# Kernel optimization log

Hardware: AMD Instinct MI355X
Metric: run time of the kernel (lower is better)

Reference implementation:

```python
import jax, jax.numpy as jnp
import numpy as np

N_NODES = 100000
N_EDGES = 1600000
IN_CH = 128


def _sage_conv(x, src, dst, Wl, b, Wr, n_nodes):
    # PyG SAGEConv (aggr='mean', root_weight=True):
    #   out_i = lin_l(mean_{j->i} x_j) + lin_r(x_i)
    msg = x[src]                                             # [E, F]
    agg = jax.ops.segment_sum(msg, dst, num_segments=n_nodes)  # [N, F]
    deg = jax.ops.segment_sum(jnp.ones((src.shape[0],), x.dtype), dst,
                              num_segments=n_nodes)          # [N]
    mean = agg / jnp.maximum(deg, 1.0)[:, None]
    return mean @ Wl + b + x @ Wr


def setup_inputs() -> dict:
    key = jax.random.key(0)
    ks = jax.random.split(key, 10)
    x = jax.random.normal(ks[0], (N_NODES, IN_CH), dtype=jnp.float32)
    edge_index = jax.random.randint(ks[1], (2, N_EDGES), 0, N_NODES, dtype=jnp.int64)
    s = 0.05
    return {
        "x": x,
        "edge_index": edge_index,
        "W1l": jax.random.normal(ks[2], (IN_CH, 32), dtype=jnp.float32) * s,
        "b1": jax.random.normal(ks[3], (32,), dtype=jnp.float32) * s,
        "W1r": jax.random.normal(ks[4], (IN_CH, 32), dtype=jnp.float32) * s,
        "W2l": jax.random.normal(ks[5], (32, 16), dtype=jnp.float32) * s,
        "b2": jax.random.normal(ks[6], (16,), dtype=jnp.float32) * s,
        "W2r": jax.random.normal(ks[7], (32, 16), dtype=jnp.float32) * s,
        "Wfc": jax.random.normal(ks[8], (16, 2), dtype=jnp.float32) * s,
        "bfc": jax.random.normal(ks[9], (2,), dtype=jnp.float32) * s,
    }


def reference(x, edge_index, W1l, b1, W1r, W2l, b2, W2r, Wfc, bfc):
    src, dst = edge_index[0], edge_index[1]
    n = x.shape[0]
    h = jax.nn.relu(_sage_conv(x, src, dst, W1l, b1, W1r, n))   # [N, 32]
    h = jax.nn.relu(_sage_conv(h, src, dst, W2l, b2, W2r, n))   # [N, 16]
    return h @ Wfc + bfc                                        # [N, 2]
```

## Files before the change

### kernel.cpp

```cpp
#include <hip/hip_runtime.h>

#define TPB 256
#define BK_SHIFT 7
#define BK_SIZE 128
#define NBK_MAX 784
#define CAP 2816
#define SC_EPB 4096
#define GEMM_BLKS 1024

typedef __attribute__((ext_vector_type(8))) short bf16x8;
typedef __attribute__((ext_vector_type(4))) float f32x4;
typedef __attribute__((ext_vector_type(2))) float f32x2;
typedef __attribute__((ext_vector_type(4))) unsigned short u16x4;

__device__ __forceinline__ unsigned short f2bf(float f) {
    unsigned u = __float_as_uint(f);
    unsigned r = (u + 0x7FFFu + ((u >> 16) & 1u)) >> 16;
    return (unsigned short)r;
}
__device__ __forceinline__ float bf2f(unsigned short b) {
    return __uint_as_float((unsigned)b << 16);
}
__device__ __forceinline__ void acc4(f32x4& a, u16x4 v) {
    a.x += bf2f(v.x); a.y += bf2f(v.y); a.z += bf2f(v.z); a.w += bf2f(v.w);
}
__device__ __forceinline__ unsigned char f2fp8(float f) {
    int p = __builtin_amdgcn_cvt_pk_fp8_f32(f, f, 0, false);
    return (unsigned char)(p & 0xFF);
}
__device__ __forceinline__ void acc4f8(f32x4& a, unsigned u) {
    f32x2 lo = __builtin_amdgcn_cvt_pk_f32_fp8(u, false);
    f32x2 hi = __builtin_amdgcn_cvt_pk_f32_fp8(u, true);
    a.x += lo.x; a.y += lo.y; a.z += hi.x; a.w += hi.y;
}
__device__ __forceinline__ void gload_lds16(const void* g, void* l) {
    __builtin_amdgcn_global_load_lds(
        (const __attribute__((address_space(1))) void*)g,
        (__attribute__((address_space(3))) void*)l, 16, 0, 0);
}

struct ScatterSmem {
    int lcnt [NBK_MAX];
    int soff [1024];
    int lbase[NBK_MAX];
    int lrank[NBK_MAX];
    int spv  [SC_EPB];
    unsigned short sbk[SC_EPB];
};
union BuildSmem {
    ScatterSmem sc;
    char xstage[4 * 8192];
};

__global__ __launch_bounds__(256) void build_and_gemm1(
    const int* __restrict__ src, const int* __restrict__ dst,
    int* __restrict__ gfill, int* __restrict__ pk, int E, int NBK, int NSC,
    const float* __restrict__ A,
    const float* __restrict__ Wl,
    const float* __restrict__ Wr,
    const float* __restrict__ b,
    unsigned char* __restrict__ Y8,
    float* __restrict__ C,
    int N)
{
    __shared__ BuildSmem smem;
    const int t = threadIdx.x;

    if ((int)blockIdx.x < NSC) {
        int* lcnt  = smem.sc.lcnt;
        int* soff  = smem.sc.soff;
        int* lbase = smem.sc.lbase;
        int* lrank = smem.sc.lrank;
        int* spv   = smem.sc.spv;
        unsigned short* sbk = smem.sc.sbk;
        const int e0 = blockIdx.x * SC_EPB;

        for (int i = t; i < NBK_MAX; i += 256) { lcnt[i] = 0; lrank[i] = 0; }
        __syncthreads();

        #pragma unroll
        for (int k = 0; k < SC_EPB / 1024; ++k) {
            int e = e0 + k * 1024 + t * 4;
            if (e < E) {
                int4 d = *(const int4*)&dst[e];
                atomicAdd(&lcnt[d.x >> BK_SHIFT], 1);
                atomicAdd(&lcnt[d.y >> BK_SHIFT], 1);
                atomicAdd(&lcnt[d.z >> BK_SHIFT], 1);
                atomicAdd(&lcnt[d.w >> BK_SHIFT], 1);
            }
        }
        __syncthreads();

        for (int i = t; i < 1024; i += 256) soff[i] = (i < NBK) ? lcnt[i] : 0;
        __syncthreads();
        for (int off = 1; off < 1024; off <<= 1) {
            int u0 = (t       >= off) ? soff[t       - off] : 0;
            int u1 = (t + 256 >= off) ? soff[t + 256 - off] : 0;
            int u2 = (t + 512 >= off) ? soff[t + 512 - off] : 0;
            int u3 = (t + 768 >= off) ? soff[t + 768 - off] : 0;
            __syncthreads();
            soff[t] += u0; soff[t + 256] += u1;
            soff[t + 512] += u2; soff[t + 768] += u3;
            __syncthreads();
        }

        for (int i = t; i < NBK; i += 256) {
            int c = lcnt[i];
            if (c) lbase[i] = atomicAdd(&gfill[i], c);
        }
        __syncthreads();

        #pragma unroll
        for (int k = 0; k < SC_EPB / 1024; ++k) {
            int e = e0 + k * 1024 + t * 4;
            if (e < E) {
                int4 d = *(const int4*)&dst[e];
                int4 s = *(const int4*)&src[e];
                {
                    int bb = d.x >> BK_SHIFT;
                    int pos = (soff[bb] - lcnt[bb]) + atomicAdd(&lrank[bb], 1);
                    spv[pos] = (s.x << BK_SHIFT) | (d.x & (BK_SIZE - 1));
                    sbk[pos] = (unsigned short)bb;
                }
                {
                    int bb = d.y >> BK_SHIFT;
                    int pos = (soff[bb] - lcnt[bb]) + atomicAdd(&lrank[bb], 1);
                    spv[pos] = (s.y << BK_SHIFT) | (d.y & (BK_SIZE - 1));
                    sbk[pos] = (unsigned short)bb;
                }
                {
                    int bb = d.z >> BK_SHIFT;
                    int pos = (soff[bb] - lcnt[bb]) + atomicAdd(&lrank[bb], 1);
                    spv[pos] = (s.z << BK_SHIFT) | (d.z & (BK_SIZE - 1));
                    sbk[pos] = (unsigned short)bb;
                }
                {
                    int bb = d.w >> BK_SHIFT;
                    int pos = (soff[bb] - lcnt[bb]) + atomicAdd(&lrank[bb], 1);
                    spv[pos] = (s.w << BK_SHIFT) | (d.w & (BK_SIZE - 1));
                    sbk[pos] = (unsigned short)bb;
                }
            }
        }
        __syncthreads();

        const int blockcnt = soff[NBK - 1];
        for (int i = t; i < blockcnt; i += 256) {
            int bb = sbk[i];
            int gpos = lbase[bb] + (i - (soff[bb] - lcnt[bb]));
            if (gpos < CAP) pk[(size_t)bb * CAP + gpos] = spv[i];
        }
        return;
    }

    const int lane = t & 63;
    const int wid  = t >> 6;
    const int m    = lane & 15;
    const int quad = lane >> 4;
    const int wave   = (blockIdx.x - NSC) * 4 + wid;
    const int nwaves = GEMM_BLKS * 4;
    const int ntiles = (N + 15) >> 4;

    char* xbuf = smem.xstage + wid * 8192;

    bf16x8 Bf[4][4];
    #pragma unroll
    for (int kc = 0; kc < 4; ++kc) {
        #pragma unroll
        for (int jt = 0; jt < 4; ++jt) {
            const float* W = (jt < 2) ? Wl : Wr;
            const int col = (jt & 1) * 16 + m;
            #pragma unroll
            for (int j = 0; j < 8; ++j) {
                int k = kc * 32 + quad * 8 + j;
                Bf[kc][jt][j] = (short)f2bf(W[k * 32 + col]);
            }
        }
    }

    const float bias0 = b[m];
    const float bias1 = b[16 + m];
    const int swz = m & 7;

    for (int tile = wave; tile < ntiles; tile += nwaves) {
        const char* xtile = (const char*)A + (size_t)tile * 8192;
        asm volatile("s_waitcnt lgkmcnt(0)" ::: "memory");
        #pragma unroll
        for (int i = 0; i < 8; ++i) {
            int o  = i * 1024 + lane * 16;
            int r  = o >> 9;
            int cs = (o & 511) >> 4;
            int c  = cs ^ (r & 7);
            gload_lds16(xtile + r * 512 + c * 16, xbuf + i * 1024);
        }
        asm volatile("s_waitcnt vmcnt(0)" ::: "memory");
        __builtin_amdgcn_sched_barrier(0);

        bf16x8 Af[4];
        #pragma unroll
        for (int kc = 0; kc < 4; ++kc) {
            const int c0 = kc * 8 + quad * 2;
            f32x4 v0 = *(const f32x4*)(xbuf + m * 512 + ((c0       ^ swz) << 4));
            f32x4 v1 = *(const f32x4*)(xbuf + m * 512 + (((c0 + 1) ^ swz) << 4));
            Af[kc][0] = (short)f2bf(v0.x); Af[kc][1] = (short)f2bf(v0.y);
            Af[kc][2] = (short)f2bf(v0.z); Af[kc][3] = (short)f2bf(v0.w);
            Af[kc][4] = (short)f2bf(v1.x); Af[kc][5] = (short)f2bf(v1.y);
            Af[kc][6] = (short)f2bf(v1.z); Af[kc][7] = (short)f2bf(v1.w);
        }

        f32x4 acc[4] = {{0.f,0.f,0.f,0.f},{0.f,0.f,0.f,0.f},
                        {0.f,0.f,0.f,0.f},{0.f,0.f,0.f,0.f}};
        #pragma unroll
        for (int kc = 0; kc < 4; ++kc) {
            #pragma unroll
            for (int jt = 0; jt < 4; ++jt)
                acc[jt] = __builtin_amdgcn_mfma_f32_16x16x32_bf16(
                    Af[kc], Bf[kc][jt], acc[jt], 0, 0, 0);
        }

        const int node0 = tile * 16;
        const int nodeBase = node0 + quad * 4;
        #pragma unroll
        for (int reg = 0; reg < 4; ++reg) {
            const int node = nodeBase + reg;
            if (node < N) {
                Y8[(size_t)node * 32 + m]      = f2fp8(acc[0][reg]);
                Y8[(size_t)node * 32 + 16 + m] = f2fp8(acc[1][reg]);
                C [(size_t)node * 32 + m]      = acc[2][reg] + bias0;
                C [(size_t)node * 32 + 16 + m] = acc[3][reg] + bias1;
            }
        }
    }
}

__global__ __launch_bounds__(256) void gather_gemm2(
    const int* __restrict__ gfill, const int* __restrict__ pk,
    const unsigned char* __restrict__ Y8,
    const float* __restrict__ c1,
    const float* __restrict__ W2l, const float* __restrict__ W2r,
    const float* __restrict__ b2,
    unsigned short* __restrict__ y2b, float* __restrict__ c2, int N)
{
    __shared__ int lcnt[BK_SIZE];
    __shared__ int soff[BK_SIZE];
    __shared__ int wcur[BK_SIZE];
    __shared__ int sidx[CAP];

    const int t = threadIdx.x;
    const int b = blockIdx.x;
    const size_t base = (size_t)b * CAP;
    const int cnt  = min(gfill[b], CAP);
    const int node0 = b * BK_SIZE;

    if (t < BK_SIZE) lcnt[t] = 0;
    __syncthreads();

    for (int j = t; j < cnt; j += 256)
        atomicAdd(&lcnt[pk[base + j] & (BK_SIZE - 1)], 1);
    __syncthreads();

    int v = (t < BK_SIZE) ? lcnt[t] : 0;
    if (t < BK_SIZE) soff[t] = v;
    __syncthreads();
    for (int off = 1; off < BK_SIZE; off <<= 1) {
        int u = (t < BK_SIZE && t >= off) ? soff[t - off] : 0;
        __syncthreads();
        if (t < BK_SIZE) soff[t] += u;
        __syncthreads();
    }
    if (t < BK_SIZE) wcur[t] = soff[t] - v;
    __syncthreads();

    for (int j = t; j < cnt; j += 256) {
        int pv = pk[base + j];
        int d  = pv & (BK_SIZE - 1);
        int pos = atomicAdd(&wcur[d], 1);
        sidx[pos] = pv >> BK_SHIFT;
    }
    __syncthreads();

    const int q = t & 7;
    #pragma unroll
    for (int pass = 0; pass < 4; ++pass) {
        const int nl = pass * 32 + (t >> 3);
        const int node = node0 + nl;
        const bool active = node < N;
        float h[4] = {0.f, 0.f, 0.f, 0.f};
        if (active) {
            const int deg = lcnt[nl];
            const int en  = soff[nl];
            const int st  = en - deg;
            const float w = 1.0f / fmaxf((float)deg, 1.0f);

            f32x4 a0 = {0.f,0.f,0.f,0.f};
            f32x4 a1 = {0.f,0.f,0.f,0.f};
            f32x4 a2 = {0.f,0.f,0.f,0.f};
            f32x4 a3 = {0.f,0.f,0.f,0.f};
            int j = st;
            for (; j + 3 < en; j += 4) {
                int s0 = sidx[j], s1 = sidx[j+1], s2 = sidx[j+2], s3 = sidx[j+3];
                unsigned u0 = *(const unsigned*)&Y8[(size_t)s0 * 32 + q * 4];
                unsigned u1 = *(const unsigned*)&Y8[(size_t)s1 * 32 + q * 4];
                unsigned u2 = *(const unsigned*)&Y8[(size_t)s2 * 32 + q * 4];
                unsigned u3 = *(const unsigned*)&Y8[(size_t)s3 * 32 + q * 4];
                acc4f8(a0, u0); acc4f8(a1, u1); acc4f8(a2, u2); acc4f8(a3, u3);
            }
            for (; j < en; ++j) {
                unsigned uu = *(const unsigned*)&Y8[(size_t)sidx[j] * 32 + q * 4];
                acc4f8(a0, uu);
            }
            f32x4 acc;
            acc.x = (a0.x + a1.x) + (a2.x + a3.x);
            acc.y = (a0.y + a1.y) + (a2.y + a3.y);
            acc.z = (a0.z + a1.z) + (a2.z + a3.z);
            acc.w = (a0.w + a1.w) + (a2.w + a3.w);

            f32x4 c = __builtin_nontemporal_load((const f32x4*)&c1[(size_t)node * 32 + q * 4]);
            h[0] = fmaxf(c.x + acc.x * w, 0.f);
            h[1] = fmaxf(c.y + acc.y * w, 0.f);
            h[2] = fmaxf(c.z + acc.z * w, 0.f);
            h[3] = fmaxf(c.w + acc.w * w, 0.f);
        }

        const int  j0  = q * 4;
        const bool isY = (j0 < 16);
        const int  jj  = isY ? j0 : (j0 - 16);
        const float* Wb = isY ? W2l : W2r;

        float o0 = 0.f, o1 = 0.f, o2 = 0.f, o3 = 0.f;
        #pragma unroll
        for (int k = 0; k < 32; ++k) {
            float hk = __shfl(h[k & 3], k >> 2, 8);
            f32x4 wv = *(const f32x4*)&Wb[k * 16 + jj];
            o0 += hk * wv.x; o1 += hk * wv.y; o2 += hk * wv.z; o3 += hk * wv.w;
        }

        if (active) {
            if (isY) {
                u16x4 r;
                r.x = f2bf(o0); r.y = f2bf(o1); r.z = f2bf(o2); r.w = f2bf(o3);
                *(u16x4*)&y2b[(size_t)node * 16 + jj] = r;
            } else {
                f32x4 bb = *(const f32x4*)&b2[jj];
                f32x4 ov = {o0 + bb.x, o1 + bb.y, o2 + bb.z, o3 + bb.w};
                __builtin_nontemporal_store(ov, (f32x4*)&c2[(size_t)node * 16 + jj]);
            }
        }
    }
}

__global__ __launch_bounds__(256) void gather_final(
    const int* __restrict__ gfill, const int* __restrict__ pk,
    const unsigned short* __restrict__ Yb,
    const float* __restrict__ c2,
    const float* __restrict__ Wfc,
    const float* __restrict__ bfc,
    float* __restrict__ out, int N)
{
    __shared__ int lcnt[BK_SIZE];
    __shared__ int soff[BK_SIZE];
    __shared__ int wcur[BK_SIZE];
    __shared__ int sidx[CAP];

    const int t = threadIdx.x;
    const int b = blockIdx.x;
    const size_t base = (size_t)b * CAP;
    const int cnt  = min(gfill[b], CAP);
    const int node0 = b * BK_SIZE;

    if (t < BK_SIZE) lcnt[t] = 0;
    __syncthreads();

    for (int j = t; j < cnt; j += 256)
        atomicAdd(&lcnt[pk[base + j] & (BK_SIZE - 1)], 1);
    __syncthreads();

    int v = (t < BK_SIZE) ? lcnt[t] : 0;
    if (t < BK_SIZE) soff[t] = v;
    __syncthreads();
    for (int off = 1; off < BK_SIZE; off <<= 1) {
        int u = (t < BK_SIZE && t >= off) ? soff[t - off] : 0;
        __syncthreads();
        if (t < BK_SIZE) soff[t] += u;
        __syncthreads();
    }
    if (t < BK_SIZE) wcur[t] = soff[t] - v;
    __syncthreads();

    for (int j = t; j < cnt; j += 256) {
        int pv = pk[base + j];
        int d  = pv & (BK_SIZE - 1);
        int pos = atomicAdd(&wcur[d], 1);
        sidx[pos] = pv >> BK_SHIFT;
    }
    __syncthreads();

    const int q = t & 3;
    #pragma unroll
    for (int pass = 0; pass < 2; ++pass) {
        const int nl = pass * 64 + (t >> 2);
        const int node = node0 + nl;
        if (node < N) {
            const int deg = lcnt[nl];
            const int en  = soff[nl];
            const int st  = en - deg;
            const float w = 1.0f / fmaxf((float)deg, 1.0f);

            f32x4 a0 = {0.f,0.f,0.f,0.f};
            f32x4 a1 = {0.f,0.f,0.f,0.f};
            f32x4 a2 = {0.f,0.f,0.f,0.f};
            f32x4 a3 = {0.f,0.f,0.f,0.f};
            int j = st;
            for (; j + 3 < en; j += 4) {
                int s0 = sidx[j], s1 = sidx[j+1], s2 = sidx[j+2], s3 = sidx[j+3];
                acc4(a0, *(const u16x4*)&Yb[(size_t)s0 * 16 + q * 4]);
                acc4(a1, *(const u16x4*)&Yb[(size_t)s1 * 16 + q * 4]);
                acc4(a2, *(const u16x4*)&Yb[(size_t)s2 * 16 + q * 4]);
                acc4(a3, *(const u16x4*)&Yb[(size_t)s3 * 16 + q * 4]);
            }
            for (; j < en; ++j)
                acc4(a0, *(const u16x4*)&Yb[(size_t)sidx[j] * 16 + q * 4]);
            f32x4 acc;
            acc.x = (a0.x + a1.x) + (a2.x + a3.x);
            acc.y = (a0.y + a1.y) + (a2.y + a3.y);
            acc.z = (a0.z + a1.z) + (a2.z + a3.z);
            acc.w = (a0.w + a1.w) + (a2.w + a3.w);

            f32x4 c = __builtin_nontemporal_load((const f32x4*)&c2[(size_t)node * 16 + q * 4]);
            float h0 = fmaxf(c.x + acc.x * w, 0.f);
            float h1 = fmaxf(c.y + acc.y * w, 0.f);
            float h2 = fmaxf(c.z + acc.z * w, 0.f);
            float h3 = fmaxf(c.w + acc.w * w, 0.f);

            const float* Wq = &Wfc[q * 8];
            float o0 = h0 * Wq[0] + h1 * Wq[2] + h2 * Wq[4] + h3 * Wq[6];
            float o1 = h0 * Wq[1] + h1 * Wq[3] + h2 * Wq[5] + h3 * Wq[7];

            o0 += __shfl_xor(o0, 1); o0 += __shfl_xor(o0, 2);
            o1 += __shfl_xor(o1, 1); o1 += __shfl_xor(o1, 2);

            if (q == 0) {
                f32x2 ov = {o0 + bfc[0], o1 + bfc[1]};
                __builtin_nontemporal_store(ov, (f32x2*)&out[(size_t)node * 2]);
            }
        } else {
            float z = 0.f;
            z += __shfl_xor(z, 1); z += __shfl_xor(z, 2);
        }
    }
}

extern "C" void kernel_launch(void* const* d_in, const int* in_sizes, int n_in,
                              void* d_out, int out_size, void* d_ws, size_t ws_size,
                              hipStream_t stream)
{
    const float* x   = (const float*)d_in[0];
    const int*   ei  = (const int*)d_in[1];
    const float* W1l = (const float*)d_in[2];
    const float* b1  = (const float*)d_in[3];
    const float* W1r = (const float*)d_in[4];
    const float* W2l = (const float*)d_in[5];
    const float* b2  = (const float*)d_in[6];
    const float* W2r = (const float*)d_in[7];
    const float* Wfc = (const float*)d_in[8];
    const float* bfc = (const float*)d_in[9];
    float* out = (float*)d_out;

    const int N = in_sizes[0] / 128;
    const int E = in_sizes[1] / 2;
    const int* src = ei;
    const int* dst = ei + E;

    const int NBK = (N + BK_SIZE - 1) / BK_SIZE;
    const int NSC = (E + SC_EPB - 1) / SC_EPB;

    int*   gfill = (int*)d_ws;
    int*   pk    = gfill + NBK_MAX + 16;
    unsigned char* y1f8 = (unsigned char*)(pk + (size_t)NBK_MAX * CAP);
    float* c1          = (float*)(y1f8 + (size_t)N * 32);
    unsigned short* y2b = (unsigned short*)(c1 + (size_t)N * 32);
    float* c2          = (float*)(y2b + (size_t)N * 16);

    hipMemsetAsync(gfill, 0, (size_t)(NBK_MAX + 16) * sizeof(int), stream);

    build_and_gemm1<<<NSC + GEMM_BLKS, TPB, 0, stream>>>(
        src, dst, gfill, pk, E, NBK, NSC,
        x, W1l, W1r, b1, y1f8, c1, N);

    gather_gemm2<<<NBK, TPB, 0, stream>>>(
        gfill, pk, y1f8, c1, W2l, W2r, b2, y2b, c2, N);

    gather_final<<<NBK, TPB, 0, stream>>>(
        gfill, pk, y2b, c2, Wfc, bfc, out, N);
}
```

Baseline: 187.3 us.

## Persist sorted CSR from gather_gemm2 so gather_final skips the rebucketing

gather_gemm2 now writes its locally sorted source indices back into the bucket array pk, plus a packed per-node (end offset, degree) word into a new nmeta buffer. gather_final drops its own shared-memory histogram, scan and scatter and reads indices and metadata straight from global memory. This removes duplicated sort work and the LDS footprint in the last kernel, which may raise occupancy. It costs extra global writes in gather_gemm2, and the index reads in gather_final now come from global/L2 instead of LDS. The nontemporal load of c2 is also swapped for a plain load.

```diff
diff --git a/kernel.cpp b/kernel.cpp
--- a/kernel.cpp
+++ b/kernel.cpp
@@ -234,12 +234,13 @@
 }
 
 __global__ __launch_bounds__(256) void gather_gemm2(
-    const int* __restrict__ gfill, const int* __restrict__ pk,
+    const int* __restrict__ gfill, int* __restrict__ pk,
     const unsigned char* __restrict__ Y8,
     const float* __restrict__ c1,
     const float* __restrict__ W2l, const float* __restrict__ W2r,
     const float* __restrict__ b2,
-    unsigned short* __restrict__ y2b, float* __restrict__ c2, int N)
+    unsigned short* __restrict__ y2b, float* __restrict__ c2,
+    int* __restrict__ nmeta, int N)
 {
     __shared__ int lcnt[BK_SIZE];
     __shared__ int soff[BK_SIZE];
@@ -278,6 +279,8 @@
         sidx[pos] = pv >> BK_SHIFT;
     }
     __syncthreads();
+
+    for (int j = t; j < cnt; j += 256) pk[base + j] = sidx[j];
 
     const int q = t & 7;
     #pragma unroll
@@ -291,6 +294,7 @@
             const int en  = soff[nl];
             const int st  = en - deg;
             const float w = 1.0f / fmaxf((float)deg, 1.0f);
+            if (q == 0) nmeta[node] = (en << 16) | deg;
 
             f32x4 a0 = {0.f,0.f,0.f,0.f};
             f32x4 a1 = {0.f,0.f,0.f,0.f};
@@ -350,50 +354,17 @@
 }
 
 __global__ __launch_bounds__(256) void gather_final(
-    const int* __restrict__ gfill, const int* __restrict__ pk,
+    const int* __restrict__ nmeta, const int* __restrict__ pk,
     const unsigned short* __restrict__ Yb,
     const float* __restrict__ c2,
     const float* __restrict__ Wfc,
     const float* __restrict__ bfc,
     float* __restrict__ out, int N)
 {
-    __shared__ int lcnt[BK_SIZE];
-    __shared__ int soff[BK_SIZE];
-    __shared__ int wcur[BK_SIZE];
-    __shared__ int sidx[CAP];
-
     const int t = threadIdx.x;
     const int b = blockIdx.x;
     const size_t base = (size_t)b * CAP;
-    const int cnt  = min(gfill[b], CAP);
     const int node0 = b * BK_SIZE;
-
-    if (t < BK_SIZE) lcnt[t] = 0;
-    __syncthreads();
-
-    for (int j = t; j < cnt; j += 256)
-        atomicAdd(&lcnt[pk[base + j] & (BK_SIZE - 1)], 1);
-    __syncthreads();
-
-    int v = (t < BK_SIZE) ? lcnt[t] : 0;
-    if (t < BK_SIZE) soff[t] = v;
-    __syncthreads();
-    for (int off = 1; off < BK_SIZE; off <<= 1) {
-        int u = (t < BK_SIZE && t >= off) ? soff[t - off] : 0;
-        __syncthreads();
-        if (t < BK_SIZE) soff[t] += u;
-        __syncthreads();
-    }
-    if (t < BK_SIZE) wcur[t] = soff[t] - v;
-    __syncthreads();
-
-    for (int j = t; j < cnt; j += 256) {
-        int pv = pk[base + j];
-        int d  = pv & (BK_SIZE - 1);
-        int pos = atomicAdd(&wcur[d], 1);
-        sidx[pos] = pv >> BK_SHIFT;
-    }
-    __syncthreads();
 
     const int q = t & 3;
     #pragma unroll
@@ -401,8 +372,9 @@
         const int nl = pass * 64 + (t >> 2);
         const int node = node0 + nl;
         if (node < N) {
-            const int deg = lcnt[nl];
-            const int en  = soff[nl];
+            const int md  = nmeta[node];
+            const int deg = md & 0xFFFF;
+            const int en  = md >> 16;
             const int st  = en - deg;
             const float w = 1.0f / fmaxf((float)deg, 1.0f);
 
@@ -412,21 +384,22 @@
             f32x4 a3 = {0.f,0.f,0.f,0.f};
             int j = st;
             for (; j + 3 < en; j += 4) {
-                int s0 = sidx[j], s1 = sidx[j+1], s2 = sidx[j+2], s3 = sidx[j+3];
+                int s0 = pk[base + j],     s1 = pk[base + j + 1];
+                int s2 = pk[base + j + 2], s3 = pk[base + j + 3];
                 acc4(a0, *(const u16x4*)&Yb[(size_t)s0 * 16 + q * 4]);
                 acc4(a1, *(const u16x4*)&Yb[(size_t)s1 * 16 + q * 4]);
                 acc4(a2, *(const u16x4*)&Yb[(size_t)s2 * 16 + q * 4]);
                 acc4(a3, *(const u16x4*)&Yb[(size_t)s3 * 16 + q * 4]);
             }
             for (; j < en; ++j)
-                acc4(a0, *(const u16x4*)&Yb[(size_t)sidx[j] * 16 + q * 4]);
+                acc4(a0, *(const u16x4*)&Yb[(size_t)pk[base + j] * 16 + q * 4]);
             f32x4 acc;
             acc.x = (a0.x + a1.x) + (a2.x + a3.x);
             acc.y = (a0.y + a1.y) + (a2.y + a3.y);
             acc.z = (a0.z + a1.z) + (a2.z + a3.z);
             acc.w = (a0.w + a1.w) + (a2.w + a3.w);
 
-            f32x4 c = __builtin_nontemporal_load((const f32x4*)&c2[(size_t)node * 16 + q * 4]);
+            f32x4 c = *(const f32x4*)&c2[(size_t)node * 16 + q * 4];
             float h0 = fmaxf(c.x + acc.x * w, 0.f);
             float h1 = fmaxf(c.y + acc.y * w, 0.f);
             float h2 = fmaxf(c.z + acc.z * w, 0.f);
@@ -480,6 +453,7 @@
     float* c1          = (float*)(y1f8 + (size_t)N * 32);
     unsigned short* y2b = (unsigned short*)(c1 + (size_t)N * 32);
     float* c2          = (float*)(y2b + (size_t)N * 16);
+    int*   nmeta       = (int*)(c2 + (size_t)N * 16);
 
     hipMemsetAsync(gfill, 0, (size_t)(NBK_MAX + 16) * sizeof(int), stream);
 
@@ -488,8 +462,8 @@
         x, W1l, W1r, b1, y1f8, c1, N);
 
     gather_gemm2<<<NBK, TPB, 0, stream>>>(
-        gfill, pk, y1f8, c1, W2l, W2r, b2, y2b, c2, N);
+        gfill, pk, y1f8, c1, W2l, W2r, b2, y2b, c2, nmeta, N);
 
     gather_final<<<NBK, TPB, 0, stream>>>(
-        gfill, pk, y2b, c2, Wfc, bfc, out, N);
-}
+        nmeta, pk, y2b, c2, Wfc, bfc, out, N);
+}
```

After: 187.5 us. Within noise of the previous version (+0.1%).
